# Kernel tuning notes

Measured on AMD Instinct MI355X. Metric: run time of the kernel, lower is better.

The kernel has to match this reference:

```python
import jax, jax.numpy as jnp
import numpy as np

N_BINS = 15
NUM_CLASSES = 16


def _risk_from_H2(u):
    # torch: 0.5*(1 - sqrt(clamp(2*2^-u - 1, min=0)))
    inner = 2.0 * jnp.exp2(-u) - 1.0
    pos = inner > 0.0
    s = jnp.sqrt(jnp.where(pos, inner, 1.0))  # safe sqrt (grad 0 where clamped)
    return 0.5 * (1.0 - jnp.where(pos, s, 0.0))


def setup_inputs() -> dict:
    key = jax.random.key(0)
    k1, k2 = jax.random.split(key)
    N = 4194304
    logits = jax.random.normal(k1, (N, NUM_CLASSES), dtype=jnp.float32)
    labels = jax.random.randint(k2, (N,), 0, NUM_CLASSES)
    return {"logits": logits, "labels": labels}


def reference(logits, labels):
    # logits: [N, C]; labels: [N]
    probs = jax.nn.softmax(logits, axis=-1)                     # [N, C]
    H2 = -jnp.log2((probs * probs).sum(-1) + 1e-12)             # [N]
    err_real = (jnp.argmax(probs, axis=-1) != labels).astype(H2.dtype)  # [N]

    # equal-frequency edges on detached H2 (linear-interp quantiles, as torch.quantile)
    q = jnp.linspace(0.0, 1.0, N_BINS + 1)
    edges = jnp.quantile(jax.lax.stop_gradient(H2), q)
    edges = edges.at[-1].add(1e-6)
    lo, hi = edges[:-1], edges[1:]                              # [n_bins]

    # vectorized replacement of the per-bin Python loop: [n_bins, N] mask
    mask = (H2[None, :] > lo[:, None]) & (H2[None, :] <= hi[:, None])
    maskf = mask.astype(H2.dtype)
    cnt = maskf.sum(-1)                                         # [n_bins]
    safe = jnp.maximum(cnt, 1.0)
    u_bar = (maskf @ H2) / safe                                 # masked means
    err_bar = (maskf @ err_real) / safe
    gaps = jnp.where(cnt > 0.0, jnp.abs(err_bar - _risk_from_H2(u_bar)), 0.0)
    return gaps.mean()
```

## Files before the change

kernel.cpp:

```cpp
#include <hip/hip_runtime.h>

#define HIST1_BINS 8320
#define KEY_CLAMP 0x40800000u
#define H1_REPL 16
#define NBIN_BLOCKS 256

struct Ranks { unsigned int r[32]; };
struct Fracs { float f[16]; };

__global__ __launch_bounds__(256) void k_h2(const float* __restrict__ logits,
                                            const int* __restrict__ labels,
                                            float* __restrict__ h2out,
                                            unsigned char* __restrict__ errout,
                                            unsigned int* __restrict__ hist1,
                                            int n) {
  __shared__ unsigned int lh[HIST1_BINS];
  for (int i = threadIdx.x; i < HIST1_BINS; i += blockDim.x) lh[i] = 0u;
  __syncthreads();
  int stride = gridDim.x * blockDim.x;
  for (int row = blockIdx.x * blockDim.x + threadIdx.x; row < n; row += stride) {
    const float4* rp = reinterpret_cast<const float4*>(logits) + (size_t)row * 4;
    float4 f0 = rp[0], f1 = rp[1], f2 = rp[2], f3 = rp[3];
    float l[16] = {f0.x, f0.y, f0.z, f0.w, f1.x, f1.y, f1.z, f1.w,
                   f2.x, f2.y, f2.z, f2.w, f3.x, f3.y, f3.z, f3.w};
    float m = l[0]; int am = 0;
#pragma unroll
    for (int j = 1; j < 16; ++j) { bool g = l[j] > m; m = g ? l[j] : m; am = g ? j : am; }
    float Z = 0.f, S2 = 0.f;
#pragma unroll
    for (int j = 0; j < 16; ++j) { float e = __expf(l[j] - m); Z += e; S2 += e * e; }
    float r = S2 / (Z * Z) + 1e-12f;
    float h2 = -__log2f(r);
    h2out[row] = h2;
    errout[row] = (unsigned char)((am != labels[row]) ? 1 : 0);
    unsigned int key = __float_as_uint(fmaxf(h2, 0.0f));
    key = key > KEY_CLAMP ? KEY_CLAMP : key;
    atomicAdd(&lh[key >> 17], 1u);
  }
  __syncthreads();
  unsigned int rep = blockIdx.x & (H1_REPL - 1);
  for (int i = threadIdx.x; i < HIST1_BINS; i += blockDim.x) {
    unsigned int v = lh[i];
    if (v) atomicAdd(&hist1[rep * HIST1_BINS + i], v);
  }
}

__global__ void k_merge(const unsigned int* __restrict__ rep,
                        unsigned int* __restrict__ merged, int nb) {
  int i = blockIdx.x * blockDim.x + threadIdx.x;
  if (i < nb) {
    unsigned int s = 0;
#pragma unroll
    for (int r = 0; r < H1_REPL; ++r) s += rep[r * nb + i];
    merged[i] = s;
  }
}

__global__ void k_select(const unsigned int* __restrict__ hist,
                         unsigned int* __restrict__ selpfx,
                         unsigned int* __restrict__ selrank,
                         float* __restrict__ vout,
                         int nb, int perq, int shift, int last, int first,
                         Ranks rk) {
  int j = blockIdx.x;
  int lane = threadIdx.x;
  const unsigned int* h = hist + (perq ? (size_t)j * (size_t)nb : (size_t)0);
  unsigned int rem = first ? rk.r[j] : selrank[j];
  int base = 0, len = nb;
  while (len > 64) {
    int chunk = (len + 63) >> 6;
    int start = base + lane * chunk;
    int end = base + len;
    unsigned int s = 0;
    for (int t = 0; t < chunk; ++t) {
      int idx = start + t;
      if (idx < end) s += h[idx];
    }
    unsigned int inc = s;
#pragma unroll
    for (int d = 1; d < 64; d <<= 1) {
      unsigned int u = __shfl_up(inc, d);
      if (lane >= d) inc += u;
    }
    unsigned int ex = inc - s;
    bool own = (rem >= ex) && (rem < ex + s);
    unsigned long long bal = __ballot(own);
    int src = __ffsll((long long)bal) - 1;
    unsigned int exs = __shfl(ex, src);
    int nbase = base + src * chunk;
    len = min(chunk, end - nbase);
    base = nbase;
    rem -= exs;
  }
  unsigned int s = (lane < len) ? h[base + lane] : 0u;
  unsigned int inc = s;
#pragma unroll
  for (int d = 1; d < 64; d <<= 1) {
    unsigned int u = __shfl_up(inc, d);
    if (lane >= d) inc += u;
  }
  unsigned int ex = inc - s;
  bool own = (rem >= ex) && (rem < ex + s);
  unsigned long long bal = __ballot(own);
  int src = __ffsll((long long)bal) - 1;
  unsigned int exs = __shfl(ex, src);
  if (lane == 0) {
    unsigned int idx = (unsigned int)(base + src);
    unsigned int pfx = first ? idx : ((selpfx[j] << shift) | idx);
    selpfx[j] = pfx;
    selrank[j] = rem - exs;
    if (last) vout[j] = __uint_as_float(pfx);
  }
}

__global__ __launch_bounds__(256) void k_refine(const float* __restrict__ h2arr,
                                                const unsigned int* __restrict__ selpfx,
                                                unsigned int* __restrict__ hist2,
                                                int n, int keyshift, int subshift,
                                                unsigned int submask, int nb) {
  __shared__ unsigned int sp[32];
  if (threadIdx.x < 32) sp[threadIdx.x] = selpfx[threadIdx.x];
  __syncthreads();
  int stride = gridDim.x * blockDim.x;
  for (int i = blockIdx.x * blockDim.x + threadIdx.x; i < n; i += stride) {
    unsigned int key = __float_as_uint(fmaxf(h2arr[i], 0.0f));
    key = key > KEY_CLAMP ? KEY_CLAMP : key;
    unsigned int hi = key >> keyshift;
    unsigned int sub = (key >> subshift) & submask;
#pragma unroll
    for (int jj = 0; jj < 32; ++jj) {
      if (hi == sp[jj]) atomicAdd(&hist2[jj * nb + (int)sub], 1u);
    }
  }
}

__global__ void k_edges(const float* __restrict__ v, float* __restrict__ edges,
                        Fracs fr) {
  int i = threadIdx.x;
  if (i < 16) {
    float lo = v[2 * i], hi = v[2 * i + 1];
    float f = fr.f[i];
    float e = lo * (1.0f - f) + hi * f;
    if (i == 15) e += 1e-6f;
    edges[i] = e;
  }
}

__global__ __launch_bounds__(256) void k_bin(const float* __restrict__ h2arr,
                                             const unsigned char* __restrict__ errarr,
                                             const float* __restrict__ edges,
                                             float* __restrict__ partials, int n) {
  __shared__ float swacc[4][48];
  float e[16];
#pragma unroll
  for (int j = 0; j < 16; ++j) e[j] = edges[j];
  float cnt[15], sH[15], sE[15];
#pragma unroll
  for (int b = 0; b < 15; ++b) { cnt[b] = 0.f; sH[b] = 0.f; sE[b] = 0.f; }
  int stride = gridDim.x * blockDim.x;
  for (int i = blockIdx.x * blockDim.x + threadIdx.x; i < n; i += stride) {
    float h = h2arr[i];
    float er = (float)errarr[i];
    int less = 0;
#pragma unroll
    for (int j = 0; j < 16; ++j) less += (h > e[j]) ? 1 : 0;
    int bin = less - 1;
#pragma unroll
    for (int b = 0; b < 15; ++b) {
      bool m = (bin == b);
      cnt[b] += m ? 1.f : 0.f;
      sH[b] += m ? h : 0.f;
      sE[b] += m ? er : 0.f;
    }
  }
  int wid = threadIdx.x >> 6;
  int lane = threadIdx.x & 63;
#pragma unroll
  for (int b = 0; b < 15; ++b) {
    float c = cnt[b], a = sH[b], s = sE[b];
    for (int off = 32; off > 0; off >>= 1) {
      c += __shfl_xor(c, off);
      a += __shfl_xor(a, off);
      s += __shfl_xor(s, off);
    }
    if (lane == 0) {
      swacc[wid][b] = c;
      swacc[wid][15 + b] = a;
      swacc[wid][30 + b] = s;
    }
  }
  __syncthreads();
  if (threadIdx.x < 45) {
    int v = threadIdx.x;
    float s = swacc[0][v] + swacc[1][v] + swacc[2][v] + swacc[3][v];
    partials[v * NBIN_BLOCKS + blockIdx.x] = s;
  }
}

__global__ void k_final(const float* __restrict__ partials, float* __restrict__ out) {
  __shared__ float sacc[45];
  int lane = threadIdx.x;
  for (int v = 0; v < 45; ++v) {
    float s = 0.f;
    for (int b = lane; b < NBIN_BLOCKS; b += 64) s += partials[v * NBIN_BLOCKS + b];
    for (int off = 32; off > 0; off >>= 1) s += __shfl_xor(s, off);
    if (lane == 0) sacc[v] = s;
  }
  __syncthreads();
  float g = 0.f;
  if (lane < 15) {
    float c = sacc[lane], sh = sacc[15 + lane], se = sacc[30 + lane];
    float safe = fmaxf(c, 1.f);
    float u = sh / safe, eb = se / safe;
    float inner = 2.0f * exp2f(-u) - 1.0f;
    float s = (inner > 0.f) ? sqrtf(inner) : 0.f;
    float risk = 0.5f * (1.0f - s);
    g = (c > 0.f) ? fabsf(eb - risk) : 0.f;
  }
  for (int off = 32; off > 0; off >>= 1) g += __shfl_xor(g, off);
  if (lane == 0) out[0] = g * (1.0f / 15.0f);
}

extern "C" void kernel_launch(void* const* d_in, const int* in_sizes, int n_in,
                              void* d_out, int out_size, void* d_ws, size_t ws_size,
                              hipStream_t stream) {
  const float* logits = (const float*)d_in[0];
  const int* labels = (const int*)d_in[1];
  float* out = (float*)d_out;
  int n = in_sizes[1];

  char* ws = (char*)d_ws;
  size_t offH2 = 0;
  size_t offErr = (size_t)n * 4;
  size_t offCtrl = (offErr + (size_t)n + 255) & ~(size_t)255;
  size_t offH1 = offCtrl;
  size_t offH1m = offH1 + (size_t)H1_REPL * HIST1_BINS * 4;
  size_t offH2a = offH1m + (size_t)HIST1_BINS * 4;
  size_t offH2b = offH2a + 32 * 512 * 4;
  size_t offSelP = offH2b + 32 * 256 * 4;
  size_t offSelR = offSelP + 128;
  size_t offV = offSelR + 128;
  size_t offE = offV + 128;
  size_t ctrlEnd = offE + 64;
  size_t offPart = (ctrlEnd + 255) & ~(size_t)255;

  float* h2p = (float*)(ws + offH2);
  unsigned char* errp = (unsigned char*)(ws + offErr);
  unsigned int* hist1 = (unsigned int*)(ws + offH1);
  unsigned int* hist1m = (unsigned int*)(ws + offH1m);
  unsigned int* h2a = (unsigned int*)(ws + offH2a);
  unsigned int* h2b = (unsigned int*)(ws + offH2b);
  unsigned int* selp = (unsigned int*)(ws + offSelP);
  unsigned int* selr = (unsigned int*)(ws + offSelR);
  float* vp = (float*)(ws + offV);
  float* edg = (float*)(ws + offE);
  float* part = (float*)(ws + offPart);

  hipMemsetAsync(ws + offCtrl, 0, ctrlEnd - offCtrl, stream);

  Ranks rk;
  Fracs fr;
  float nm1 = (float)(n - 1);
  for (int i = 0; i < 16; ++i) {
    float q = (i == 15) ? 1.0f : (float)i * (1.0f / 15.0f);
    float idxf = q * nm1;
    float flo = floorf(idxf);
    unsigned int klo = (unsigned int)flo;
    unsigned int khi = (unsigned int)ceilf(idxf);
    unsigned int maxi = (unsigned int)(n - 1);
    if (klo > maxi) klo = maxi;
    if (khi > maxi) khi = maxi;
    rk.r[2 * i] = klo;
    rk.r[2 * i + 1] = khi;
    fr.f[i] = idxf - flo;
  }

  k_h2<<<1024, 256, 0, stream>>>(logits, labels, h2p, errp, hist1, n);
  k_merge<<<(HIST1_BINS + 255) / 256, 256, 0, stream>>>(hist1, hist1m, HIST1_BINS);
  k_select<<<32, 64, 0, stream>>>(hist1m, selp, selr, vp, HIST1_BINS, 0, 0, 0, 1, rk);
  k_refine<<<1024, 256, 0, stream>>>(h2p, selp, h2a, n, 17, 8, 0x1FFu, 512);
  k_select<<<32, 64, 0, stream>>>(h2a, selp, selr, vp, 512, 1, 9, 0, 0, rk);
  k_refine<<<1024, 256, 0, stream>>>(h2p, selp, h2b, n, 8, 0, 0xFFu, 256);
  k_select<<<32, 64, 0, stream>>>(h2b, selp, selr, vp, 256, 1, 8, 1, 0, rk);
  k_edges<<<1, 64, 0, stream>>>(vp, edg, fr);
  k_bin<<<NBIN_BLOCKS, 256, 0, stream>>>(h2p, errp, edg, part, n);
  k_final<<<1, 64, 0, stream>>>(part, out);

  (void)n_in; (void)out_size; (void)ws_size;
}
```

Before: 352.2 us.

## Quantize H2 to fixed-point keys packed with error bit, two-level radix select

H2 values are quantized to 22-bit fixed-point keys (scale 2^20) with the misclassification flag packed into the top bit, so one 4-byte array replaces the float and byte arrays. The quantile search drops from three radix levels to two, removing one full refine pass over the data. Per-block histograms are written as packed 16-bit pairs and merged without global atomics, and the memset and edge kernels are folded into a zero kernel and k_bin. The cost is that H2 becomes a quantized approximation (resolution about 1e-6), which can move samples across bin edges or change the edges compared with the exact float computation.

```diff
diff --git a/kernel.cpp b/kernel.cpp
--- a/kernel.cpp
+++ b/kernel.cpp
@@ -1,21 +1,26 @@
 #include <hip/hip_runtime.h>
 
-#define HIST1_BINS 8320
-#define KEY_CLAMP 0x40800000u
-#define H1_REPL 16
+#define L1_BINS 8192
+#define L2_BINS 512
+#define KEY_MAX 4194303u
+#define NH2_BLOCKS 1024
 #define NBIN_BLOCKS 256
 
 struct Ranks { unsigned int r[32]; };
 struct Fracs { float f[16]; };
 
+__global__ __launch_bounds__(256) void k_zero(uint4* __restrict__ p, int n4) {
+  int i = blockIdx.x * blockDim.x + threadIdx.x;
+  if (i < n4) p[i] = make_uint4(0u, 0u, 0u, 0u);
+}
+
 __global__ __launch_bounds__(256) void k_h2(const float* __restrict__ logits,
                                             const int* __restrict__ labels,
-                                            float* __restrict__ h2out,
-                                            unsigned char* __restrict__ errout,
-                                            unsigned int* __restrict__ hist1,
+                                            unsigned int* __restrict__ keys,
+                                            unsigned int* __restrict__ histg,
                                             int n) {
-  __shared__ unsigned int lh[HIST1_BINS];
-  for (int i = threadIdx.x; i < HIST1_BINS; i += blockDim.x) lh[i] = 0u;
+  __shared__ unsigned int lh[L1_BINS];
+  for (int i = threadIdx.x; i < L1_BINS; i += blockDim.x) lh[i] = 0u;
   __syncthreads();
   int stride = gridDim.x * blockDim.x;
   for (int row = blockIdx.x * blockDim.x + threadIdx.x; row < n; row += stride) {
@@ -31,28 +36,31 @@
     for (int j = 0; j < 16; ++j) { float e = __expf(l[j] - m); Z += e; S2 += e * e; }
     float r = S2 / (Z * Z) + 1e-12f;
     float h2 = -__log2f(r);
-    h2out[row] = h2;
-    errout[row] = (unsigned char)((am != labels[row]) ? 1 : 0);
-    unsigned int key = __float_as_uint(fmaxf(h2, 0.0f));
-    key = key > KEY_CLAMP ? KEY_CLAMP : key;
-    atomicAdd(&lh[key >> 17], 1u);
-  }
-  __syncthreads();
-  unsigned int rep = blockIdx.x & (H1_REPL - 1);
-  for (int i = threadIdx.x; i < HIST1_BINS; i += blockDim.x) {
-    unsigned int v = lh[i];
-    if (v) atomicAdd(&hist1[rep * HIST1_BINS + i], v);
-  }
-}
-
-__global__ void k_merge(const unsigned int* __restrict__ rep,
-                        unsigned int* __restrict__ merged, int nb) {
+    int ki = (int)(h2 * 1048576.0f);
+    unsigned int key = (unsigned int)min(max(ki, 0), (int)KEY_MAX);
+    unsigned int err = (am != labels[row]) ? 0x80000000u : 0u;
+    keys[row] = key | err;
+    atomicAdd(&lh[key >> 9], 1u);
+  }
+  __syncthreads();
+  unsigned int* dst = histg + (size_t)blockIdx.x * (L1_BINS / 2);
+  for (int i = threadIdx.x; i < L1_BINS / 2; i += blockDim.x)
+    dst[i] = (lh[2 * i] & 0xFFFFu) | (lh[2 * i + 1] << 16);
+}
+
+__global__ __launch_bounds__(256) void k_merge(const unsigned int* __restrict__ histg,
+                                               unsigned int* __restrict__ merged,
+                                               int nblocks) {
   int i = blockIdx.x * blockDim.x + threadIdx.x;
-  if (i < nb) {
-    unsigned int s = 0;
-#pragma unroll
-    for (int r = 0; r < H1_REPL; ++r) s += rep[r * nb + i];
-    merged[i] = s;
+  if (i < L1_BINS / 2) {
+    unsigned int slo = 0, shi = 0;
+    for (int b = 0; b < nblocks; ++b) {
+      unsigned int v = histg[(size_t)b * (L1_BINS / 2) + i];
+      slo += v & 0xFFFFu;
+      shi += v >> 16;
+    }
+    merged[2 * i] = slo;
+    merged[2 * i + 1] = shi;
   }
 }
 
@@ -113,54 +121,54 @@
   }
 }
 
-__global__ __launch_bounds__(256) void k_refine(const float* __restrict__ h2arr,
+__global__ __launch_bounds__(256) void k_refine(const unsigned int* __restrict__ keys,
                                                 const unsigned int* __restrict__ selpfx,
                                                 unsigned int* __restrict__ hist2,
-                                                int n, int keyshift, int subshift,
-                                                unsigned int submask, int nb) {
+                                                int n) {
   __shared__ unsigned int sp[32];
   if (threadIdx.x < 32) sp[threadIdx.x] = selpfx[threadIdx.x];
   __syncthreads();
   int stride = gridDim.x * blockDim.x;
   for (int i = blockIdx.x * blockDim.x + threadIdx.x; i < n; i += stride) {
-    unsigned int key = __float_as_uint(fmaxf(h2arr[i], 0.0f));
-    key = key > KEY_CLAMP ? KEY_CLAMP : key;
-    unsigned int hi = key >> keyshift;
-    unsigned int sub = (key >> subshift) & submask;
+    unsigned int key = keys[i] & KEY_MAX;
+    unsigned int hi = key >> 9;
+    unsigned int sub = key & (L2_BINS - 1);
 #pragma unroll
     for (int jj = 0; jj < 32; ++jj) {
-      if (hi == sp[jj]) atomicAdd(&hist2[jj * nb + (int)sub], 1u);
-    }
-  }
-}
-
-__global__ void k_edges(const float* __restrict__ v, float* __restrict__ edges,
-                        Fracs fr) {
-  int i = threadIdx.x;
-  if (i < 16) {
-    float lo = v[2 * i], hi = v[2 * i + 1];
+      if (hi == sp[jj]) atomicAdd(&hist2[jj * L2_BINS + (int)sub], 1u);
+    }
+  }
+}
+
+__global__ __launch_bounds__(256) void k_bin(const unsigned int* __restrict__ keys,
+                                             const float* __restrict__ vp,
+                                             float* __restrict__ partials, int n,
+                                             Fracs fr) {
+  __shared__ float sedge[16];
+  __shared__ float swacc[4][48];
+  if (threadIdx.x < 16) {
+    int i = threadIdx.x;
+    unsigned int klo = __float_as_uint(vp[2 * i]);
+    unsigned int khi = __float_as_uint(vp[2 * i + 1]);
+    float lo = (float)(klo + 1u) * 0x1p-20f;
+    float hi = (float)(khi + 1u) * 0x1p-20f;
     float f = fr.f[i];
     float e = lo * (1.0f - f) + hi * f;
     if (i == 15) e += 1e-6f;
-    edges[i] = e;
-  }
-}
-
-__global__ __launch_bounds__(256) void k_bin(const float* __restrict__ h2arr,
-                                             const unsigned char* __restrict__ errarr,
-                                             const float* __restrict__ edges,
-                                             float* __restrict__ partials, int n) {
-  __shared__ float swacc[4][48];
+    sedge[i] = e;
+  }
+  __syncthreads();
   float e[16];
 #pragma unroll
-  for (int j = 0; j < 16; ++j) e[j] = edges[j];
+  for (int j = 0; j < 16; ++j) e[j] = sedge[j];
   float cnt[15], sH[15], sE[15];
 #pragma unroll
   for (int b = 0; b < 15; ++b) { cnt[b] = 0.f; sH[b] = 0.f; sE[b] = 0.f; }
   int stride = gridDim.x * blockDim.x;
   for (int i = blockIdx.x * blockDim.x + threadIdx.x; i < n; i += stride) {
-    float h = h2arr[i];
-    float er = (float)errarr[i];
+    unsigned int kp = keys[i];
+    float h = ((float)(kp & KEY_MAX) + 0.5f) * 0x1p-20f;
+    float er = (kp & 0x80000000u) ? 1.0f : 0.0f;
     int less = 0;
 #pragma unroll
     for (int j = 0; j < 16; ++j) less += (h > e[j]) ? 1 : 0;
@@ -230,33 +238,23 @@
   int n = in_sizes[1];
 
   char* ws = (char*)d_ws;
-  size_t offH2 = 0;
-  size_t offErr = (size_t)n * 4;
-  size_t offCtrl = (offErr + (size_t)n + 255) & ~(size_t)255;
-  size_t offH1 = offCtrl;
-  size_t offH1m = offH1 + (size_t)H1_REPL * HIST1_BINS * 4;
-  size_t offH2a = offH1m + (size_t)HIST1_BINS * 4;
-  size_t offH2b = offH2a + 32 * 512 * 4;
-  size_t offSelP = offH2b + 32 * 256 * 4;
+  size_t offKeys = 0;
+  size_t offHg = (size_t)n * 4;
+  size_t offMerged = offHg + (size_t)NH2_BLOCKS * (L1_BINS / 2) * 4;
+  size_t offH2b = offMerged + (size_t)L1_BINS * 4;
+  size_t offSelP = offH2b + 32 * L2_BINS * 4;
   size_t offSelR = offSelP + 128;
   size_t offV = offSelR + 128;
-  size_t offE = offV + 128;
-  size_t ctrlEnd = offE + 64;
-  size_t offPart = (ctrlEnd + 255) & ~(size_t)255;
-
-  float* h2p = (float*)(ws + offH2);
-  unsigned char* errp = (unsigned char*)(ws + offErr);
-  unsigned int* hist1 = (unsigned int*)(ws + offH1);
-  unsigned int* hist1m = (unsigned int*)(ws + offH1m);
-  unsigned int* h2a = (unsigned int*)(ws + offH2a);
-  unsigned int* h2b = (unsigned int*)(ws + offH2b);
+  size_t offPart = (offV + 128 + 255) & ~(size_t)255;
+
+  unsigned int* keys = (unsigned int*)(ws + offKeys);
+  unsigned int* histg = (unsigned int*)(ws + offHg);
+  unsigned int* merged = (unsigned int*)(ws + offMerged);
+  unsigned int* hist2 = (unsigned int*)(ws + offH2b);
   unsigned int* selp = (unsigned int*)(ws + offSelP);
   unsigned int* selr = (unsigned int*)(ws + offSelR);
   float* vp = (float*)(ws + offV);
-  float* edg = (float*)(ws + offE);
   float* part = (float*)(ws + offPart);
-
-  hipMemsetAsync(ws + offCtrl, 0, ctrlEnd - offCtrl, stream);
 
   Ranks rk;
   Fracs fr;
@@ -275,15 +273,13 @@
     fr.f[i] = idxf - flo;
   }
 
-  k_h2<<<1024, 256, 0, stream>>>(logits, labels, h2p, errp, hist1, n);
-  k_merge<<<(HIST1_BINS + 255) / 256, 256, 0, stream>>>(hist1, hist1m, HIST1_BINS);
-  k_select<<<32, 64, 0, stream>>>(hist1m, selp, selr, vp, HIST1_BINS, 0, 0, 0, 1, rk);
-  k_refine<<<1024, 256, 0, stream>>>(h2p, selp, h2a, n, 17, 8, 0x1FFu, 512);
-  k_select<<<32, 64, 0, stream>>>(h2a, selp, selr, vp, 512, 1, 9, 0, 0, rk);
-  k_refine<<<1024, 256, 0, stream>>>(h2p, selp, h2b, n, 8, 0, 0xFFu, 256);
-  k_select<<<32, 64, 0, stream>>>(h2b, selp, selr, vp, 256, 1, 8, 1, 0, rk);
-  k_edges<<<1, 64, 0, stream>>>(vp, edg, fr);
-  k_bin<<<NBIN_BLOCKS, 256, 0, stream>>>(h2p, errp, edg, part, n);
+  k_zero<<<16, 256, 0, stream>>>((uint4*)(ws + offH2b), 32 * L2_BINS / 4);
+  k_h2<<<NH2_BLOCKS, 256, 0, stream>>>(logits, labels, keys, histg, n);
+  k_merge<<<(L1_BINS / 2 + 255) / 256, 256, 0, stream>>>(histg, merged, NH2_BLOCKS);
+  k_select<<<32, 64, 0, stream>>>(merged, selp, selr, vp, L1_BINS, 0, 0, 0, 1, rk);
+  k_refine<<<NH2_BLOCKS, 256, 0, stream>>>(keys, selp, hist2, n);
+  k_select<<<32, 64, 0, stream>>>(hist2, selp, selr, vp, L2_BINS, 1, 9, 1, 0, rk);
+  k_bin<<<NBIN_BLOCKS, 256, 0, stream>>>(keys, vp, part, n, fr);
   k_final<<<1, 64, 0, stream>>>(part, out);
 
   (void)n_in; (void)out_size; (void)ws_size;
```

New measurement: 323.1 us. 8.3% less time.
